# Kernel tuning notes

Measured on AMD Instinct MI355X. Metric: run time of the kernel, lower is better.

Reference implementation:

```python
import jax, jax.numpy as jnp
import numpy as np

B, T, C, H = 2, 2048, 2048, 16
HD = C // H  # head dim = 128
BASE = 10000.0


def _rope_tables(seq_len, d):
    p = jnp.arange(d // 2, dtype=jnp.float32)
    # faithful to source: exponent uses 2**p (power of two), not 2*p
    theta = jnp.power(BASE, -(2.0 ** p) / d)            # [d/2]
    pos = jnp.arange(1, seq_len + 1, dtype=jnp.float32)[:, None]  # 1-indexed positions
    c = pos * theta                                      # [T, d/2]
    ang = jnp.concatenate([c, c], axis=-1)               # [T, d]
    return jnp.cos(ang), jnp.sin(ang)


def _rope(x):
    # x: [B, H, T, d]
    d = x.shape[-1]
    cos, sin = _rope_tables(x.shape[-2], d)
    half = d // 2
    x_rot = jnp.concatenate([-x[..., half:], x[..., :half]], axis=-1)
    return x * cos + x_rot * sin


def setup_inputs() -> dict:
    key = jax.random.key(0)
    k1, k2, k3 = jax.random.split(key, 3)
    x = jax.random.normal(k1, (B, T, C), dtype=jnp.float32)
    Wqkv = jax.random.normal(k2, (3 * C, C), dtype=jnp.float32) * 0.02
    bqkv = jnp.zeros((3 * C,), dtype=jnp.float32)
    Wo = jax.random.normal(k3, (C, C), dtype=jnp.float32) * 0.02
    bo = jnp.zeros((C,), dtype=jnp.float32)
    return {"x": x, "Wqkv": Wqkv, "bqkv": bqkv, "Wo": Wo, "bo": bo}


def reference(x, Wqkv, bqkv, Wo, bo):
    b, t, c = x.shape
    qkv = x @ Wqkv.T + bqkv                      # [B, T, 3C]
    q, k, v = jnp.split(qkv, 3, axis=-1)
    # [B, T, C] -> [B, H, T, HD]
    def to_heads(z):
        return z.reshape(b, t, H, HD).transpose(0, 2, 1, 3)
    q, k, v = to_heads(q), to_heads(k), to_heads(v)
    q = _rope(q)
    k = _rope(k)
    scale = 1.0 / jnp.sqrt(jnp.float32(HD))
    att = jnp.einsum('bhqd,bhkd->bhqk', q, k) * scale   # [B, H, T, T]
    causal = jnp.tril(jnp.ones((t, t), dtype=bool))
    att = jnp.where(causal, att, -jnp.inf)
    att = jax.nn.softmax(att, axis=-1)
    y = jnp.einsum('bhqk,bhkd->bhqd', att, v)           # [B, H, T, HD]
    y = y.transpose(0, 2, 1, 3).reshape(b, t, c)
    y = y @ Wo.T + bo
    return y
```

## Files before the change

### kernel.cpp

```cpp
#include <hip/hip_runtime.h>
#include <hip/hip_bf16.h>


typedef __attribute__((ext_vector_type(8))) short short8;
typedef __attribute__((ext_vector_type(4))) float f32x4;

#define B_  2
#define T_  2048
#define C_  2048
#define H_  16
#define HD_ 128

#define BARRIER() asm volatile("s_barrier" ::: "memory")
#define LGKM0()   asm volatile("s_waitcnt lgkmcnt(0)" ::: "memory")

template<int N> __device__ __forceinline__ void vmwait() {
  if constexpr (N == 6)      asm volatile("s_waitcnt vmcnt(6)" ::: "memory");
  else if constexpr (N == 3) asm volatile("s_waitcnt vmcnt(3)" ::: "memory");
  else if constexpr (N == 0) asm volatile("s_waitcnt vmcnt(0)" ::: "memory");
}

__device__ __forceinline__ float bf2f(unsigned short u) {
  union { unsigned int i; float f; } v; v.i = ((unsigned int)u) << 16; return v.f;
}
__device__ __forceinline__ unsigned short f2bf(float f) {
  union { float f; unsigned int i; } v; v.f = f;
  unsigned int x = v.i;
  return (unsigned short)((x + 0x7fffu + ((x >> 16) & 1u)) >> 16);
}
__device__ __forceinline__ float fexp2(float x) {
#if __has_builtin(__builtin_amdgcn_exp2f)
  return __builtin_amdgcn_exp2f(x);
#else
  return exp2f(x);
#endif
}

__device__ __forceinline__ void gll16(const unsigned short* g, unsigned short* lds_base) {
  __builtin_amdgcn_global_load_lds(
      (const __attribute__((address_space(1))) void*)g,
      (__attribute__((address_space(3))) void*)lds_base, 16, 0, 0);
}

__global__ void cvt_k(const float* __restrict__ src, unsigned short* __restrict__ dst, int n4)
{
  int i = blockIdx.x * blockDim.x + threadIdx.x;
  if (i < n4) {
    float4 v = ((const float4*)src)[i];
    ushort4 h;
    h.x = f2bf(v.x); h.y = f2bf(v.y); h.z = f2bf(v.z); h.w = f2bf(v.w);
    ((ushort4*)dst)[i] = h;
  }
}

template<int CB, bool S1, bool S2, int V1, int V2>
__device__ __forceinline__ void ktile(
    int t,
    const unsigned short* __restrict__ Ag,
    const unsigned short* __restrict__ Bg, int K,
    unsigned short (&LA)[2][2][128][32],
    unsigned short (&LB)[2][2][256][32],
    f32x4 (&acc)[4][4],
    int wave, int wm, int wn, int l15, int csw8, int sra, int sc)
{
  short8 af[4], bf[4];
  const int ca = sc ^ ((sra >> 1) & 3);

#pragma unroll
  for (int m = 0; m < 4; ++m)
    af[m] = *(const short8*)&LA[CB][0][wm * 64 + m * 16 + l15][csw8];
#pragma unroll
  for (int n = 0; n < 4; ++n)
    bf[n] = *(const short8*)&LB[CB][0][wn * 64 + n * 16 + l15][csw8];
  if constexpr (S1) {
    const int kb = (t + 1) * 64 + 32;
    gll16(Ag + (size_t)sra * K + kb + ca * 8,         &LA[CB ^ 1][1][wave * 16][0]);
    gll16(Bg + (size_t)sra * K + kb + ca * 8,         &LB[CB ^ 1][1][wave * 16][0]);
    gll16(Bg + (size_t)(128 + sra) * K + kb + ca * 8, &LB[CB ^ 1][1][128 + wave * 16][0]);
  }
  BARRIER();
  LGKM0();
  __builtin_amdgcn_s_setprio(1);
#pragma unroll
  for (int m = 0; m < 4; ++m)
#pragma unroll
    for (int n = 0; n < 4; ++n)
      acc[m][n] = __builtin_amdgcn_mfma_f32_16x16x32_bf16(af[m], bf[n], acc[m][n], 0, 0, 0);
  __builtin_amdgcn_s_setprio(0);
  vmwait<V1>();
  BARRIER();

#pragma unroll
  for (int m = 0; m < 4; ++m)
    af[m] = *(const short8*)&LA[CB][1][wm * 64 + m * 16 + l15][csw8];
#pragma unroll
  for (int n = 0; n < 4; ++n)
    bf[n] = *(const short8*)&LB[CB][1][wn * 64 + n * 16 + l15][csw8];
  if constexpr (S2) {
    const int kb = (t + 2) * 64;
    gll16(Ag + (size_t)sra * K + kb + ca * 8,         &LA[CB][0][wave * 16][0]);
    gll16(Bg + (size_t)sra * K + kb + ca * 8,         &LB[CB][0][wave * 16][0]);
    gll16(Bg + (size_t)(128 + sra) * K + kb + ca * 8, &LB[CB][0][128 + wave * 16][0]);
  }
  BARRIER();
  LGKM0();
  __builtin_amdgcn_s_setprio(1);
#pragma unroll
  for (int m = 0; m < 4; ++m)
#pragma unroll
    for (int n = 0; n < 4; ++n)
      acc[m][n] = __builtin_amdgcn_mfma_f32_16x16x32_bf16(af[m], bf[n], acc[m][n], 0, 0, 0);
  __builtin_amdgcn_s_setprio(0);
  vmwait<V2>();
  BARRIER();
}

template<int MODE>
__global__ __launch_bounds__(512, 2)
void gemm128(const unsigned short* __restrict__ A,
             const unsigned short* __restrict__ Bw,
             const float* __restrict__ bias,
             float* __restrict__ Cout,
             unsigned short* __restrict__ Qb,
             unsigned short* __restrict__ Kb,
             unsigned short* __restrict__ Vb,
             int N, int K)
{
  __shared__ unsigned short LA[2][2][128][32];
  __shared__ unsigned short LB[2][2][256][32];

  const int tid  = threadIdx.x;
  const int wave = tid >> 6, lane = tid & 63;
  const int quad = lane >> 4, l15 = lane & 15;
  const int wm = wave >> 2, wn = wave & 3;
  const int csw8 = (quad ^ ((l15 >> 1) & 3)) * 8;
  const int sra = tid >> 2, sc = tid & 3;

  const int n0 = blockIdx.x * 256;
  const int m0 = blockIdx.y * 128;

  const unsigned short* Ag = A  + (size_t)m0 * K;
  const unsigned short* Bg = Bw + (size_t)n0 * K;

  f32x4 acc[4][4];
#pragma unroll
  for (int i = 0; i < 4; i++)
#pragma unroll
    for (int j = 0; j < 4; j++) acc[i][j] = (f32x4){0.f, 0.f, 0.f, 0.f};

  {
    const int ca = sc ^ ((sra >> 1) & 3);
    gll16(Ag + (size_t)sra * K + ca * 8,              &LA[0][0][wave * 16][0]);
    gll16(Bg + (size_t)sra * K + ca * 8,              &LB[0][0][wave * 16][0]);
    gll16(Bg + (size_t)(128 + sra) * K + ca * 8,      &LB[0][0][128 + wave * 16][0]);
    gll16(Ag + (size_t)sra * K + 32 + ca * 8,         &LA[0][1][wave * 16][0]);
    gll16(Bg + (size_t)sra * K + 32 + ca * 8,         &LB[0][1][wave * 16][0]);
    gll16(Bg + (size_t)(128 + sra) * K + 32 + ca * 8, &LB[0][1][128 + wave * 16][0]);
    gll16(Ag + (size_t)sra * K + 64 + ca * 8,         &LA[1][0][wave * 16][0]);
    gll16(Bg + (size_t)sra * K + 64 + ca * 8,         &LB[1][0][wave * 16][0]);
    gll16(Bg + (size_t)(128 + sra) * K + 64 + ca * 8, &LB[1][0][128 + wave * 16][0]);
    asm volatile("s_waitcnt vmcnt(6)" ::: "memory");
    BARRIER();
  }

  const int NT = K >> 6;
#pragma unroll 1
  for (int t = 0; t + 2 < NT; t += 2) {
    ktile<0, true, true, 6, 6>(t,     Ag, Bg, K, LA, LB, acc, wave, wm, wn, l15, csw8, sra, sc);
    ktile<1, true, true, 6, 6>(t + 1, Ag, Bg, K, LA, LB, acc, wave, wm, wn, l15, csw8, sra, sc);
  }
  ktile<0, true,  false, 6,  3>(NT - 2, Ag, Bg, K, LA, LB, acc, wave, wm, wn, l15, csw8, sra, sc);
  ktile<1, false, false, 0, -1>(NT - 1, Ag, Bg, K, LA, LB, acc, wave, wm, wn, l15, csw8, sra, sc);

  if constexpr (MODE == 0) {
#pragma unroll
    for (int mi = 0; mi < 4; mi++)
#pragma unroll
      for (int n = 0; n < 4; n++) {
        int col = n0 + wn * 64 + n * 16 + l15;
        float bv = bias[col];
#pragma unroll
        for (int r = 0; r < 4; r++) {
          int row = m0 + wm * 64 + mi * 16 + quad * 4 + r;
          Cout[(size_t)row * N + col] = acc[mi][n][r] + bv;
        }
      }
  } else {
    const int which = n0 >> 11;
    unsigned short* P = (which == 0) ? Qb : (which == 1) ? Kb : Vb;
#pragma unroll
    for (int mi = 0; mi < 4; mi++)
#pragma unroll
      for (int n = 0; n < 4; n++) {
        int col = n0 + wn * 64 + n * 16 + l15;
        float bv = bias[col];
        int h = (col >> 7) & 15, d = col & 127;
#pragma unroll
        for (int r = 0; r < 4; r++) {
          int m = m0 + wm * 64 + mi * 16 + quad * 4 + r;
          int b = m >> 11, t = m & (T_ - 1);
          size_t addr = (which == 2)
              ? ((size_t)((b * H_ + h) * HD_ + d)) * T_ + t
              : ((size_t)((b * H_ + h) * T_ + t)) * HD_ + d;
          P[addr] = f2bf(acc[mi][n][r] + bv);
        }
      }
  }
}

__global__ void rope_k(unsigned short* __restrict__ Q, unsigned short* __restrict__ K)
{
  const int tid = threadIdx.x;
  const int w = tid >> 6, l = tid & 63;
  const int r = blockIdx.x * 4 + w;
  const int t = r & (T_ - 1);
  const float pos = (float)(t + 1);
  const float theta = expf(-exp2f((float)l) * 0.07195578415606394f);
  const float ang = pos * theta;
  const float c = cosf(ang), s = sinf(ang);
  const float QS = 0.08838834764831845f * 1.4426950408889634f;
  const size_t base = (size_t)r * HD_;

  float q0 = bf2f(Q[base + l]), q1 = bf2f(Q[base + l + 64]);
  Q[base + l]      = f2bf((q0 * c - q1 * s) * QS);
  Q[base + l + 64] = f2bf((q1 * c + q0 * s) * QS);
  float k0 = bf2f(K[base + l]), k1 = bf2f(K[base + l + 64]);
  K[base + l]      = f2bf(k0 * c - k1 * s);
  K[base + l + 64] = f2bf(k1 * c + k0 * s);
}

__global__ __launch_bounds__(256, 2)
void attn_k(const unsigned short* __restrict__ Q,
            const unsigned short* __restrict__ K,
            const unsigned short* __restrict__ Vt_g,
            unsigned short* __restrict__ AO)
{
  __shared__ unsigned short Kl[64 * 128];
  __shared__ unsigned short Vl[128 * 64];
  __shared__ unsigned short Pl[4 * 16 * 72];

  const int tid  = threadIdx.x;
  const int wave = tid >> 6, lane = tid & 63;
  const int quad = lane >> 4, l15 = lane & 15;
  const int blk = blockIdx.x;
  const int bh = (blk & 7) + 8 * ((blk >> 3) & 3);
  const int qp = (blk >> 5) & 15;
  const unsigned short* Qh = Q    + (size_t)bh * T_ * HD_;
  const unsigned short* Kh = K    + (size_t)bh * T_ * HD_;
  const unsigned short* Vh = Vt_g + (size_t)bh * T_ * HD_;
  const int b = bh >> 4, h = bh & 15;

#pragma unroll
  for (int tile = 0; tile < 2; tile++) {
    const int q0 = (tile == 0 ? qp : 31 - qp) * 64;
    const int wq = q0 + wave * 16;
    short8 qf[4];
#pragma unroll
    for (int kc = 0; kc < 4; kc++)
      qf[kc] = *(const short8*)&Qh[(size_t)(wq + l15) * HD_ + kc * 32 + quad * 8];

    f32x4 oacc[8];
#pragma unroll
    for (int n = 0; n < 8; n++) oacc[n] = (f32x4){0.f, 0.f, 0.f, 0.f};
    float mst[4], lst[4];
#pragma unroll
    for (int r = 0; r < 4; r++) { mst[r] = -1e30f; lst[r] = 0.f; }

    const int niter = (q0 >> 6) + 1;
    for (int it = 0; it < niter; it++) {
      const int kt = it * 64;
      __syncthreads();
#pragma unroll
      for (int i = 0; i < 4; i++) {
        int cc = i * 256 + wave * 64 + lane;
        int kr = cc >> 4, kcs = (cc & 15) ^ (kr & 15);
        gll16(Kh + (size_t)(kt + kr) * HD_ + kcs * 8, &Kl[(i * 4 + wave) * 512]);
        int vr = cc >> 3, vcs = (cc & 7) ^ (vr & 7);
        gll16(Vh + (size_t)vr * T_ + kt + vcs * 8, &Vl[(i * 4 + wave) * 512]);
      }
      __syncthreads();

      f32x4 sa[4];
#pragma unroll
      for (int ni = 0; ni < 4; ni++) sa[ni] = (f32x4){0.f, 0.f, 0.f, 0.f};
#pragma unroll
      for (int kc = 0; kc < 4; kc++) {
        const int cswK = (((kc * 4 + quad) ^ l15) * 8);
        short8 bfr[4];
#pragma unroll
        for (int ni = 0; ni < 4; ni++)
          bfr[ni] = *(const short8*)&Kl[(ni * 16 + l15) * HD_ + cswK];
#pragma unroll
        for (int ni = 0; ni < 4; ni++)
          sa[ni] = __builtin_amdgcn_mfma_f32_16x16x32_bf16(qf[kc], bfr[ni], sa[ni], 0, 0, 0);
      }

      if (kt == q0) {
#pragma unroll
        for (int ni = 0; ni < 4; ni++) {
          int gcol = kt + ni * 16 + l15;
#pragma unroll
          for (int r = 0; r < 4; r++) {
            int grow = wq + quad * 4 + r;
            if (gcol > grow) sa[ni][r] = -1e30f;
          }
        }
      }

      float rmax[4] = {-1e30f, -1e30f, -1e30f, -1e30f};
#pragma unroll
      for (int ni = 0; ni < 4; ni++)
#pragma unroll
        for (int r = 0; r < 4; r++) rmax[r] = fmaxf(rmax[r], sa[ni][r]);
#pragma unroll
      for (int r = 0; r < 4; r++)
#pragma unroll
        for (int off = 1; off < 16; off <<= 1)
          rmax[r] = fmaxf(rmax[r], __shfl_xor(rmax[r], off));
      float alpha[4];
#pragma unroll
      for (int r = 0; r < 4; r++) {
        float mnew = fmaxf(mst[r], rmax[r]);
        alpha[r] = fexp2(fminf(mst[r] - mnew, 0.f));
        mst[r] = mnew;
      }
      float rsum[4] = {0.f, 0.f, 0.f, 0.f};
#pragma unroll
      for (int ni = 0; ni < 4; ni++)
#pragma unroll
        for (int r = 0; r < 4; r++) {
          float p = fexp2(fminf(sa[ni][r] - mst[r], 0.f));
          sa[ni][r] = p;
          rsum[r] += p;
        }
#pragma unroll
      for (int r = 0; r < 4; r++) {
#pragma unroll
        for (int off = 1; off < 16; off <<= 1)
          rsum[r] += __shfl_xor(rsum[r], off);
        lst[r] = lst[r] * alpha[r] + rsum[r];
      }
#pragma unroll
      for (int nv = 0; nv < 8; nv++)
#pragma unroll
        for (int r = 0; r < 4; r++) oacc[nv][r] *= alpha[r];
#pragma unroll
      for (int ni = 0; ni < 4; ni++)
#pragma unroll
        for (int r = 0; r < 4; r++)
          Pl[wave * 16 * 72 + (quad * 4 + r) * 72 + ni * 16 + l15] = f2bf(sa[ni][r]);
      __syncthreads();

      short8 pf[2];
#pragma unroll
      for (int kc = 0; kc < 2; kc++)
        pf[kc] = *(const short8*)&Pl[wave * 16 * 72 + l15 * 72 + kc * 32 + quad * 8];
#pragma unroll
      for (int kc = 0; kc < 2; kc++) {
        const int cswV = (((kc * 4 + quad) ^ (l15 & 7)) * 8);
#pragma unroll
        for (int nv = 0; nv < 8; nv++) {
          short8 vb = *(const short8*)&Vl[(nv * 16 + l15) * 64 + cswV];
          oacc[nv] = __builtin_amdgcn_mfma_f32_16x16x32_bf16(pf[kc], vb, oacc[nv], 0, 0, 0);
        }
      }
    }

    float linv[4];
#pragma unroll
    for (int r = 0; r < 4; r++) linv[r] = 1.0f / fmaxf(lst[r], 1e-20f);
#pragma unroll
    for (int nv = 0; nv < 8; nv++)
#pragma unroll
      for (int r = 0; r < 4; r++) {
        int t = wq + quad * 4 + r;
        int d = nv * 16 + l15;
        AO[((size_t)(b * T_ + t)) * C_ + h * HD_ + d] = f2bf(oacc[nv][r] * linv[r]);
      }
  }
}

template<int A32, int B32, int MODE>
__global__ __launch_bounds__(256, 2)
void gemm_nt(const void* __restrict__ Ap, const void* __restrict__ Bp,
             const float* __restrict__ bias,
             float* __restrict__ Cout,
             unsigned short* __restrict__ Qb,
             unsigned short* __restrict__ Kb,
             unsigned short* __restrict__ Vb,
             int N, int K)
{
  __shared__ unsigned short Al[128 * 72];
  __shared__ unsigned short Bl[128 * 72];
  const int tid  = threadIdx.x;
  const int wave = tid >> 6, lane = tid & 63;
  const int quad = lane >> 4, l15 = lane & 15;
  const int wm = wave >> 1, wn = wave & 1;
  const int n0 = blockIdx.x * 128, m0 = blockIdx.y * 128;

  f32x4 acc[4][4];
#pragma unroll
  for (int i = 0; i < 4; i++)
#pragma unroll
    for (int j = 0; j < 4; j++) acc[i][j] = (f32x4){0.f, 0.f, 0.f, 0.f};

  for (int k0 = 0; k0 < K; k0 += 64) {
    __syncthreads();
    if constexpr (A32) {
      const float* A = (const float*)Ap;
#pragma unroll
      for (int i = 0; i < 8; i++) {
        int cid = tid + i * 256;
        int r = cid >> 4, c = cid & 15;
        float4 v = *(const float4*)&A[(size_t)(m0 + r) * K + k0 + c * 4];
        ushort4 hh;
        hh.x = f2bf(v.x); hh.y = f2bf(v.y); hh.z = f2bf(v.z); hh.w = f2bf(v.w);
        *(ushort4*)&Al[r * 72 + c * 4] = hh;
      }
    } else {
      const unsigned short* A = (const unsigned short*)Ap;
#pragma unroll
      for (int i = 0; i < 4; i++) {
        int cid = tid + i * 256;
        int r = cid >> 3, c = cid & 7;
        *(float4*)&Al[r * 72 + c * 8] =
            *(const float4*)&A[(size_t)(m0 + r) * K + k0 + c * 8];
      }
    }
    if constexpr (B32) {
      const float* Bm = (const float*)Bp;
#pragma unroll
      for (int i = 0; i < 8; i++) {
        int cid = tid + i * 256;
        int r = cid >> 4, c = cid & 15;
        float4 v = *(const float4*)&Bm[(size_t)(n0 + r) * K + k0 + c * 4];
        ushort4 hh;
        hh.x = f2bf(v.x); hh.y = f2bf(v.y); hh.z = f2bf(v.z); hh.w = f2bf(v.w);
        *(ushort4*)&Bl[r * 72 + c * 4] = hh;
      }
    } else {
      const unsigned short* Bm = (const unsigned short*)Bp;
#pragma unroll
      for (int i = 0; i < 4; i++) {
        int cid = tid + i * 256;
        int r = cid >> 3, c = cid & 7;
        *(float4*)&Bl[r * 72 + c * 8] =
            *(const float4*)&Bm[(size_t)(n0 + r) * K + k0 + c * 8];
      }
    }
    __syncthreads();
#pragma unroll
    for (int kc = 0; kc < 2; kc++) {
      short8 af[4], bfr[4];
#pragma unroll
      for (int mi = 0; mi < 4; mi++)
        af[mi] = *(const short8*)&Al[(wm * 64 + mi * 16 + l15) * 72 + kc * 32 + quad * 8];
#pragma unroll
      for (int ni = 0; ni < 4; ni++)
        bfr[ni] = *(const short8*)&Bl[(wn * 64 + ni * 16 + l15) * 72 + kc * 32 + quad * 8];
#pragma unroll
      for (int mi = 0; mi < 4; mi++)
#pragma unroll
        for (int ni = 0; ni < 4; ni++)
          acc[mi][ni] = __builtin_amdgcn_mfma_f32_16x16x32_bf16(af[mi], bfr[ni], acc[mi][ni], 0, 0, 0);
    }
  }

  if constexpr (MODE == 0) {
#pragma unroll
    for (int mi = 0; mi < 4; mi++)
#pragma unroll
      for (int ni = 0; ni < 4; ni++) {
        int col = n0 + wn * 64 + ni * 16 + l15;
        float bv = bias[col];
#pragma unroll
        for (int r = 0; r < 4; r++) {
          int row = m0 + wm * 64 + mi * 16 + quad * 4 + r;
          Cout[(size_t)row * N + col] = acc[mi][ni][r] + bv;
        }
      }
  } else {
    int which = n0 >> 11;
    int h = (n0 >> 7) & 15;
    unsigned short* P = (which == 0) ? Qb : (which == 1) ? Kb : Vb;
#pragma unroll
    for (int mi = 0; mi < 4; mi++)
#pragma unroll
      for (int ni = 0; ni < 4; ni++) {
        int d = wn * 64 + ni * 16 + l15;
        float bv = bias[n0 + d];
#pragma unroll
        for (int r = 0; r < 4; r++) {
          int m = m0 + wm * 64 + mi * 16 + quad * 4 + r;
          int b = m >> 11, t = m & (T_ - 1);
          size_t addr = (which == 2)
              ? ((size_t)((b * H_ + h) * HD_ + d)) * T_ + t
              : ((size_t)((b * H_ + h) * T_ + t)) * HD_ + d;
          P[addr] = f2bf(acc[mi][ni][r] + bv);
        }
      }
  }
}

extern "C" void kernel_launch(void* const* d_in, const int* in_sizes, int n_in,
                              void* d_out, int out_size, void* d_ws, size_t ws_size,
                              hipStream_t stream)
{
  const float* x    = (const float*)d_in[0];
  const float* Wqkv = (const float*)d_in[1];
  const float* bqkv = (const float*)d_in[2];
  const float* Wo   = (const float*)d_in[3];
  const float* bo   = (const float*)d_in[4];
  float* out = (float*)d_out;

  const size_t SZ   = (size_t)B_ * H_ * T_ * HD_;
  const size_t NX   = SZ;
  const size_t NWQ  = (size_t)3 * C_ * C_;
  const size_t NWO  = (size_t)C_ * C_;
  unsigned short* ws = (unsigned short*)d_ws;

  dim3 blk(256, 1, 1);
  dim3 blk512(512, 1, 1);
  const size_t need = (NX + NWQ + 3 * SZ) * sizeof(unsigned short);

  if (ws_size >= need) {
    unsigned short* xb    = ws;
    unsigned short* Wqkvb = xb + NX;
    unsigned short* Qb    = Wqkvb + NWQ;
    unsigned short* Kb    = Qb + SZ;
    unsigned short* Vb    = Kb + SZ;
    unsigned short* AO    = xb;
    unsigned short* Wob   = Wqkvb;

    cvt_k<<<dim3((unsigned)(NX / 1024)), blk, 0, stream>>>(x, xb, (int)(NX / 4));
    cvt_k<<<dim3((unsigned)(NWQ / 1024)), blk, 0, stream>>>(Wqkv, Wqkvb, (int)(NWQ / 4));
    gemm128<1><<<dim3(24, 32, 1), blk512, 0, stream>>>(
        xb, Wqkvb, bqkv, nullptr, Qb, Kb, Vb, 6144, 2048);
    cvt_k<<<dim3((unsigned)(NWO / 1024)), blk, 0, stream>>>(Wo, Wob, (int)(NWO / 4));
    rope_k<<<dim3((B_ * H_ * T_) / 4, 1, 1), blk, 0, stream>>>(Qb, Kb);
    attn_k<<<dim3(512, 1, 1), blk, 0, stream>>>(Qb, Kb, Vb, AO);
    gemm128<0><<<dim3(8, 32, 1), blk512, 0, stream>>>(
        AO, Wob, bo, out, nullptr, nullptr, nullptr, 2048, 2048);
  } else {
    unsigned short* Qb = ws;
    unsigned short* Kb = Qb + SZ;
    unsigned short* Vb = Kb + SZ;
    unsigned short* AO = Vb + SZ;
    gemm_nt<1, 1, 1><<<dim3(48, 32, 1), blk, 0, stream>>>(
        (const void*)x, (const void*)Wqkv, bqkv, nullptr, Qb, Kb, Vb, 6144, 2048);
    rope_k<<<dim3((B_ * H_ * T_) / 4, 1, 1), blk, 0, stream>>>(Qb, Kb);
    attn_k<<<dim3(512, 1, 1), blk, 0, stream>>>(Qb, Kb, Vb, AO);
    gemm_nt<0, 1, 0><<<dim3(16, 32, 1), blk, 0, stream>>>(
        (const void*)AO, (const void*)Wo, bo, out, nullptr, nullptr, nullptr, 2048, 2048);
  }
}
```

Baseline: 434.4 us.

## Enlarge GEMM block tile to 256x256 with four-phase staged pipeline

Doubles the M dimension of the bf16 MFMA GEMM block tile from 128 to 256, so each 512-thread block accumulates an 8x4 grid of 16x16 fragments. The k-tile body is split into four MFMA phases, with A and B half-tile prefetches interleaved between them and vmcnt waits retuned to match. The goal is higher arithmetic intensity and less global/LDS traffic per FLOP. In exchange, the grids shrink to 384 blocks for the QKV projection and 128 blocks for the output projection, which can leave compute units idle or unevenly loaded. Register and LDS pressure per block also rise.

```diff
diff --git a/kernel.cpp b/kernel.cpp
--- a/kernel.cpp
+++ b/kernel.cpp
@@ -15,7 +15,9 @@
 #define LGKM0()   asm volatile("s_waitcnt lgkmcnt(0)" ::: "memory")
 
 template<int N> __device__ __forceinline__ void vmwait() {
-  if constexpr (N == 6)      asm volatile("s_waitcnt vmcnt(6)" ::: "memory");
+  if constexpr (N == 8)      asm volatile("s_waitcnt vmcnt(8)" ::: "memory");
+  else if constexpr (N == 6) asm volatile("s_waitcnt vmcnt(6)" ::: "memory");
+  else if constexpr (N == 4) asm volatile("s_waitcnt vmcnt(4)" ::: "memory");
   else if constexpr (N == 3) asm volatile("s_waitcnt vmcnt(3)" ::: "memory");
   else if constexpr (N == 0) asm volatile("s_waitcnt vmcnt(0)" ::: "memory");
 }
@@ -53,71 +55,105 @@
   }
 }
 
-template<int CB, bool S1, bool S2, int V1, int V2>
-__device__ __forceinline__ void ktile(
+__device__ __forceinline__ void stage_unit(
+    const unsigned short* __restrict__ G, int K, int t, int kk,
+    unsigned short (&L)[2][2][2][256][32], int buf, int mat,
+    int wave, int sra, int ca8)
+{
+  const unsigned short* s = G + (size_t)sra * K + t * 64 + kk * 32 + ca8;
+  gll16(s,                   &L[buf][kk][mat][wave * 16][0]);
+  gll16(s + (size_t)128 * K, &L[buf][kk][mat][128 + wave * 16][0]);
+}
+
+template<int CB, bool SN1, bool SN2, int V0, int V1, int V2, int V3>
+__device__ __forceinline__ void ktile256(
     int t,
     const unsigned short* __restrict__ Ag,
     const unsigned short* __restrict__ Bg, int K,
-    unsigned short (&LA)[2][2][128][32],
-    unsigned short (&LB)[2][2][256][32],
-    f32x4 (&acc)[4][4],
-    int wave, int wm, int wn, int l15, int csw8, int sra, int sc)
+    unsigned short (&L)[2][2][2][256][32],
+    f32x4 (&acc)[8][4],
+    int wave, int wm, int wn, int l15, int csw8, int sra, int ca8)
 {
   short8 af[4], bf[4];
-  const int ca = sc ^ ((sra >> 1) & 3);
-
-#pragma unroll
-  for (int m = 0; m < 4; ++m)
-    af[m] = *(const short8*)&LA[CB][0][wm * 64 + m * 16 + l15][csw8];
+
 #pragma unroll
   for (int n = 0; n < 4; ++n)
-    bf[n] = *(const short8*)&LB[CB][0][wn * 64 + n * 16 + l15][csw8];
-  if constexpr (S1) {
-    const int kb = (t + 1) * 64 + 32;
-    gll16(Ag + (size_t)sra * K + kb + ca * 8,         &LA[CB ^ 1][1][wave * 16][0]);
-    gll16(Bg + (size_t)sra * K + kb + ca * 8,         &LB[CB ^ 1][1][wave * 16][0]);
-    gll16(Bg + (size_t)(128 + sra) * K + kb + ca * 8, &LB[CB ^ 1][1][128 + wave * 16][0]);
-  }
+    bf[n] = *(const short8*)&L[CB][0][1][wn * 64 + n * 16 + l15][csw8];
+#pragma unroll
+  for (int j = 0; j < 4; ++j)
+    af[j] = *(const short8*)&L[CB][0][0][wm * 128 + j * 16 + l15][csw8];
+  if constexpr (SN1)
+    stage_unit(Ag, K, t + 1, 1, L, CB ^ 1, 0, wave, sra, ca8);
   BARRIER();
   LGKM0();
   __builtin_amdgcn_s_setprio(1);
 #pragma unroll
-  for (int m = 0; m < 4; ++m)
+  for (int j = 0; j < 4; ++j)
 #pragma unroll
     for (int n = 0; n < 4; ++n)
-      acc[m][n] = __builtin_amdgcn_mfma_f32_16x16x32_bf16(af[m], bf[n], acc[m][n], 0, 0, 0);
+      acc[j][n] = __builtin_amdgcn_mfma_f32_16x16x32_bf16(af[j], bf[n], acc[j][n], 0, 0, 0);
+  __builtin_amdgcn_s_setprio(0);
+  vmwait<V0>();
+  BARRIER();
+
+#pragma unroll
+  for (int j = 0; j < 4; ++j)
+    af[j] = *(const short8*)&L[CB][0][0][wm * 128 + 64 + j * 16 + l15][csw8];
+  if constexpr (SN1)
+    stage_unit(Bg, K, t + 1, 1, L, CB ^ 1, 1, wave, sra, ca8);
+  BARRIER();
+  LGKM0();
+  __builtin_amdgcn_s_setprio(1);
+#pragma unroll
+  for (int j = 0; j < 4; ++j)
+#pragma unroll
+    for (int n = 0; n < 4; ++n)
+      acc[4 + j][n] = __builtin_amdgcn_mfma_f32_16x16x32_bf16(af[j], bf[n], acc[4 + j][n], 0, 0, 0);
   __builtin_amdgcn_s_setprio(0);
   vmwait<V1>();
   BARRIER();
 
 #pragma unroll
-  for (int m = 0; m < 4; ++m)
-    af[m] = *(const short8*)&LA[CB][1][wm * 64 + m * 16 + l15][csw8];
-#pragma unroll
   for (int n = 0; n < 4; ++n)
-    bf[n] = *(const short8*)&LB[CB][1][wn * 64 + n * 16 + l15][csw8];
-  if constexpr (S2) {
-    const int kb = (t + 2) * 64;
-    gll16(Ag + (size_t)sra * K + kb + ca * 8,         &LA[CB][0][wave * 16][0]);
-    gll16(Bg + (size_t)sra * K + kb + ca * 8,         &LB[CB][0][wave * 16][0]);
-    gll16(Bg + (size_t)(128 + sra) * K + kb + ca * 8, &LB[CB][0][128 + wave * 16][0]);
-  }
+    bf[n] = *(const short8*)&L[CB][1][1][wn * 64 + n * 16 + l15][csw8];
+#pragma unroll
+  for (int j = 0; j < 4; ++j)
+    af[j] = *(const short8*)&L[CB][1][0][wm * 128 + j * 16 + l15][csw8];
+  if constexpr (SN2)
+    stage_unit(Ag, K, t + 2, 0, L, CB, 0, wave, sra, ca8);
   BARRIER();
   LGKM0();
   __builtin_amdgcn_s_setprio(1);
 #pragma unroll
-  for (int m = 0; m < 4; ++m)
+  for (int j = 0; j < 4; ++j)
 #pragma unroll
     for (int n = 0; n < 4; ++n)
-      acc[m][n] = __builtin_amdgcn_mfma_f32_16x16x32_bf16(af[m], bf[n], acc[m][n], 0, 0, 0);
+      acc[j][n] = __builtin_amdgcn_mfma_f32_16x16x32_bf16(af[j], bf[n], acc[j][n], 0, 0, 0);
   __builtin_amdgcn_s_setprio(0);
   vmwait<V2>();
   BARRIER();
+
+#pragma unroll
+  for (int j = 0; j < 4; ++j)
+    af[j] = *(const short8*)&L[CB][1][0][wm * 128 + 64 + j * 16 + l15][csw8];
+  if constexpr (SN2)
+    stage_unit(Bg, K, t + 2, 0, L, CB, 1, wave, sra, ca8);
+  BARRIER();
+  LGKM0();
+  __builtin_amdgcn_s_setprio(1);
+#pragma unroll
+  for (int j = 0; j < 4; ++j)
+#pragma unroll
+    for (int n = 0; n < 4; ++n)
+      acc[4 + j][n] = __builtin_amdgcn_mfma_f32_16x16x32_bf16(af[j], bf[n], acc[4 + j][n], 0, 0, 0);
+  __builtin_amdgcn_s_setprio(0);
+  vmwait<V3>();
+  BARRIER();
 }
 
 template<int MODE>
 __global__ __launch_bounds__(512, 2)
-void gemm128(const unsigned short* __restrict__ A,
+void gemm256(const unsigned short* __restrict__ A,
              const unsigned short* __restrict__ Bw,
              const float* __restrict__ bias,
              float* __restrict__ Cout,
@@ -126,62 +162,55 @@
              unsigned short* __restrict__ Vb,
              int N, int K)
 {
-  __shared__ unsigned short LA[2][2][128][32];
-  __shared__ unsigned short LB[2][2][256][32];
+  __shared__ unsigned short L[2][2][2][256][32];
 
   const int tid  = threadIdx.x;
   const int wave = tid >> 6, lane = tid & 63;
   const int quad = lane >> 4, l15 = lane & 15;
   const int wm = wave >> 2, wn = wave & 3;
   const int csw8 = (quad ^ ((l15 >> 1) & 3)) * 8;
-  const int sra = tid >> 2, sc = tid & 3;
+  const int sra = tid >> 2;
+  const int ca8 = ((tid & 3) ^ ((sra >> 1) & 3)) * 8;
 
   const int n0 = blockIdx.x * 256;
-  const int m0 = blockIdx.y * 128;
-
+  const int m0 = blockIdx.y * 256;
   const unsigned short* Ag = A  + (size_t)m0 * K;
   const unsigned short* Bg = Bw + (size_t)n0 * K;
 
-  f32x4 acc[4][4];
-#pragma unroll
-  for (int i = 0; i < 4; i++)
+  f32x4 acc[8][4];
+#pragma unroll
+  for (int i = 0; i < 8; i++)
 #pragma unroll
     for (int j = 0; j < 4; j++) acc[i][j] = (f32x4){0.f, 0.f, 0.f, 0.f};
 
-  {
-    const int ca = sc ^ ((sra >> 1) & 3);
-    gll16(Ag + (size_t)sra * K + ca * 8,              &LA[0][0][wave * 16][0]);
-    gll16(Bg + (size_t)sra * K + ca * 8,              &LB[0][0][wave * 16][0]);
-    gll16(Bg + (size_t)(128 + sra) * K + ca * 8,      &LB[0][0][128 + wave * 16][0]);
-    gll16(Ag + (size_t)sra * K + 32 + ca * 8,         &LA[0][1][wave * 16][0]);
-    gll16(Bg + (size_t)sra * K + 32 + ca * 8,         &LB[0][1][wave * 16][0]);
-    gll16(Bg + (size_t)(128 + sra) * K + 32 + ca * 8, &LB[0][1][128 + wave * 16][0]);
-    gll16(Ag + (size_t)sra * K + 64 + ca * 8,         &LA[1][0][wave * 16][0]);
-    gll16(Bg + (size_t)sra * K + 64 + ca * 8,         &LB[1][0][wave * 16][0]);
-    gll16(Bg + (size_t)(128 + sra) * K + 64 + ca * 8, &LB[1][0][128 + wave * 16][0]);
-    asm volatile("s_waitcnt vmcnt(6)" ::: "memory");
-    BARRIER();
-  }
+  stage_unit(Ag, K, 0, 0, L, 0, 0, wave, sra, ca8);
+  stage_unit(Bg, K, 0, 0, L, 0, 1, wave, sra, ca8);
+  stage_unit(Ag, K, 0, 1, L, 0, 0, wave, sra, ca8);
+  stage_unit(Bg, K, 0, 1, L, 0, 1, wave, sra, ca8);
+  stage_unit(Ag, K, 1, 0, L, 1, 0, wave, sra, ca8);
+  stage_unit(Bg, K, 1, 0, L, 1, 1, wave, sra, ca8);
+  vmwait<8>();
+  BARRIER();
 
   const int NT = K >> 6;
 #pragma unroll 1
-  for (int t = 0; t + 2 < NT; t += 2) {
-    ktile<0, true, true, 6, 6>(t,     Ag, Bg, K, LA, LB, acc, wave, wm, wn, l15, csw8, sra, sc);
-    ktile<1, true, true, 6, 6>(t + 1, Ag, Bg, K, LA, LB, acc, wave, wm, wn, l15, csw8, sra, sc);
-  }
-  ktile<0, true,  false, 6,  3>(NT - 2, Ag, Bg, K, LA, LB, acc, wave, wm, wn, l15, csw8, sra, sc);
-  ktile<1, false, false, 0, -1>(NT - 1, Ag, Bg, K, LA, LB, acc, wave, wm, wn, l15, csw8, sra, sc);
+  for (int t = 0; t + 3 < NT; t += 2) {
+    ktile256<0, true, true, 8, 8, 8, 8>(t,     Ag, Bg, K, L, acc, wave, wm, wn, l15, csw8, sra, ca8);
+    ktile256<1, true, true, 8, 8, 8, 8>(t + 1, Ag, Bg, K, L, acc, wave, wm, wn, l15, csw8, sra, ca8);
+  }
+  ktile256<0, true,  false, 8,  8,  8,  4>(NT - 2, Ag, Bg, K, L, acc, wave, wm, wn, l15, csw8, sra, ca8);
+  ktile256<1, false, false, -1, 0, -1, -1>(NT - 1, Ag, Bg, K, L, acc, wave, wm, wn, l15, csw8, sra, ca8);
 
   if constexpr (MODE == 0) {
 #pragma unroll
-    for (int mi = 0; mi < 4; mi++)
+    for (int mi = 0; mi < 8; mi++)
 #pragma unroll
       for (int n = 0; n < 4; n++) {
         int col = n0 + wn * 64 + n * 16 + l15;
         float bv = bias[col];
 #pragma unroll
         for (int r = 0; r < 4; r++) {
-          int row = m0 + wm * 64 + mi * 16 + quad * 4 + r;
+          int row = m0 + wm * 128 + mi * 16 + quad * 4 + r;
           Cout[(size_t)row * N + col] = acc[mi][n][r] + bv;
         }
       }
@@ -189,7 +218,7 @@
     const int which = n0 >> 11;
     unsigned short* P = (which == 0) ? Qb : (which == 1) ? Kb : Vb;
 #pragma unroll
-    for (int mi = 0; mi < 4; mi++)
+    for (int mi = 0; mi < 8; mi++)
 #pragma unroll
       for (int n = 0; n < 4; n++) {
         int col = n0 + wn * 64 + n * 16 + l15;
@@ -197,7 +226,7 @@
         int h = (col >> 7) & 15, d = col & 127;
 #pragma unroll
         for (int r = 0; r < 4; r++) {
-          int m = m0 + wm * 64 + mi * 16 + quad * 4 + r;
+          int m = m0 + wm * 128 + mi * 16 + quad * 4 + r;
           int b = m >> 11, t = m & (T_ - 1);
           size_t addr = (which == 2)
               ? ((size_t)((b * H_ + h) * HD_ + d)) * T_ + t
@@ -534,12 +563,12 @@
 
     cvt_k<<<dim3((unsigned)(NX / 1024)), blk, 0, stream>>>(x, xb, (int)(NX / 4));
     cvt_k<<<dim3((unsigned)(NWQ / 1024)), blk, 0, stream>>>(Wqkv, Wqkvb, (int)(NWQ / 4));
-    gemm128<1><<<dim3(24, 32, 1), blk512, 0, stream>>>(
+    gemm256<1><<<dim3(24, 16, 1), blk512, 0, stream>>>(
         xb, Wqkvb, bqkv, nullptr, Qb, Kb, Vb, 6144, 2048);
     cvt_k<<<dim3((unsigned)(NWO / 1024)), blk, 0, stream>>>(Wo, Wob, (int)(NWO / 4));
     rope_k<<<dim3((B_ * H_ * T_) / 4, 1, 1), blk, 0, stream>>>(Qb, Kb);
     attn_k<<<dim3(512, 1, 1), blk, 0, stream>>>(Qb, Kb, Vb, AO);
-    gemm128<0><<<dim3(8, 32, 1), blk512, 0, stream>>>(
+    gemm256<0><<<dim3(8, 16, 1), blk512, 0, stream>>>(
         AO, Wob, bo, out, nullptr, nullptr, nullptr, 2048, 2048);
   } else {
     unsigned short* Qb = ws;
```

Result: no change. 432.4 us (-0.4%).
